# Optimization experiments

Measured on AMD Instinct MI355X. Metric: run time of the kernel, lower is better.

Reference implementation:

```python
import jax, jax.numpy as jnp
import numpy as np

DIM = 1024
HEADS = 16

def setup_inputs() -> dict:
    key = jax.random.key(0)
    k1, k2, k3, k4 = jax.random.split(key, 4)
    x = jax.random.normal(k1, (2, 2048, DIM), dtype=jnp.float32)
    # torch Linear weights are [out_features, in_features]
    w_qkv = jax.random.normal(k2, (3 * DIM, DIM), dtype=jnp.float32) * (DIM ** -0.5)
    w_out = jax.random.normal(k3, (DIM, DIM), dtype=jnp.float32) * (DIM ** -0.5)
    b_out = jax.random.normal(k4, (DIM,), dtype=jnp.float32) * 0.01
    return {"x": x, "w_qkv": w_qkv, "w_out": w_out, "b_out": b_out}

def reference(x, w_qkv, w_out, b_out):
    b, n, dim = x.shape
    h = HEADS
    d = dim // h
    scale = dim ** -0.5  # NOTE: full dim, faithful to source
    qkv = x @ w_qkv.T                       # [b, n, 3*dim]
    qkv = qkv.reshape(b, n, 3, h, d)        # split (qkv h d)
    q, k, v = (qkv[:, :, i].transpose(0, 2, 1, 3) for i in range(3))  # [b, h, n, d]
    scores = jnp.einsum('bhid,bhjd->bhij', q, k) * scale
    weights = jax.nn.softmax(scores, axis=-1)
    out = jnp.einsum('bhij,bhjd->bhid', weights, v)  # [b, h, n, d]
    out = out.transpose(0, 2, 1, 3).reshape(b, n, dim)
    return out @ w_out.T + b_out
```

## Files before the change

kernel.cpp:

```cpp
#include <hip/hip_runtime.h>

#define DIM   1024
#define HEADS 16
#define NSEQ  2048
#define BATCH 2

typedef unsigned short u16;
typedef unsigned long long u64;
typedef __attribute__((ext_vector_type(8))) short bf16x8;
typedef __attribute__((ext_vector_type(4))) float f32x4;
typedef __attribute__((ext_vector_type(16))) float f32x16;

__device__ __forceinline__ u16 f2b(float f) {
  union { float f; unsigned u; } v; v.f = f;
  unsigned r = (v.u + 0x7fffu + ((v.u >> 16) & 1u)) >> 16;
  return (u16)r;
}

__device__ __forceinline__ void g2l16(const u16* g, u16* l) {
  __builtin_amdgcn_global_load_lds(
      (const __attribute__((address_space(1))) void*)g,
      (__attribute__((address_space(3))) void*)l, 16, 0, 0);
}

__global__ void cvt_bf16(const float* __restrict__ src, u16* __restrict__ dst,
                         int n4, int sc4, float s) {
  int i = blockIdx.x * blockDim.x + threadIdx.x;
  if (i < n4) {
    float4 f = ((const float4*)src)[i];
    float m = (i < sc4) ? s : 1.0f;
    union { u16 s[4]; u64 ll; } o;
    o.s[0] = f2b(f.x * m); o.s[1] = f2b(f.y * m);
    o.s[2] = f2b(f.z * m); o.s[3] = f2b(f.w * m);
    ((u64*)dst)[i] = o.ll;
  }
}

__global__ __launch_bounds__(256, 2)
void gemm_bt(const u16* __restrict__ A, const u16* __restrict__ Bt,
             void* __restrict__ C, const float* __restrict__ bias,
             int M, int Nc, int K, int bf16_out) {
  __shared__ u16 As[128 * 64];
  __shared__ u16 Bs[128 * 64];
  const int tid  = threadIdx.x;
  const int wave = tid >> 6, lane = tid & 63;
  const int l15  = lane & 15, quad = lane >> 4;
  const int m0 = blockIdx.y * 128, n0 = blockIdx.x * 128;
  const int wm = (wave >> 1) * 64, wn = (wave & 1) * 64;
  const int rb = wave * 32;

  f32x4 acc[4][4] = {};

  for (int kt = 0; kt < K; kt += 64) {
#pragma unroll
    for (int c = 0; c < 4; ++c) {
      int r  = rb + c * 8 + (lane >> 3);
      int ck = (lane & 7) ^ (r & 7);
      g2l16(A  + (size_t)(m0 + r) * K + kt + ck * 8, &As[(rb + c * 8) * 64]);
      g2l16(Bt + (size_t)(n0 + r) * K + kt + ck * 8, &Bs[(rb + c * 8) * 64]);
    }
    __syncthreads();
#pragma unroll
    for (int ks = 0; ks < 2; ++ks) {
      bf16x8 a[4], b[4];
      int ch = ks * 4 + quad;
#pragma unroll
      for (int i = 0; i < 4; ++i) {
        int ra  = wm + i * 16 + l15;
        a[i] = *(const bf16x8*)&As[ra * 64 + ((ch ^ (ra & 7)) << 3)];
        int rb2 = wn + i * 16 + l15;
        b[i] = *(const bf16x8*)&Bs[rb2 * 64 + ((ch ^ (rb2 & 7)) << 3)];
      }
#pragma unroll
      for (int i = 0; i < 4; ++i)
#pragma unroll
        for (int j = 0; j < 4; ++j)
          acc[i][j] = __builtin_amdgcn_mfma_f32_16x16x32_bf16(a[i], b[j], acc[i][j], 0, 0, 0);
    }
    __syncthreads();
  }

#pragma unroll
  for (int i = 0; i < 4; ++i)
#pragma unroll
    for (int j = 0; j < 4; ++j) {
      int row = m0 + wm + i * 16 + quad * 4;
      int col = n0 + wn + j * 16 + l15;
#pragma unroll
      for (int r = 0; r < 4; ++r) {
        float v = acc[i][j][r];
        if (bf16_out) ((u16*)C)[(size_t)(row + r) * Nc + col] = f2b(v);
        else          ((float*)C)[(size_t)(row + r) * Nc + col] = v + bias[col];
      }
    }
}

__global__ __launch_bounds__(256, 2)
void attn(const u16* __restrict__ qkv, u16* __restrict__ outp) {
  __shared__ u16 Ks[2][128 * 64];
  __shared__ u16 Vts[2][64 * 128];
  const int tid  = threadIdx.x;
  const int wave = tid >> 6, lane = tid & 63;
  const int l31  = lane & 31, h = lane >> 5;
  const int b = blockIdx.x >> 4, hd = blockIdx.x & 15;
  const int q0 = blockIdx.y * 128;
  const u16* base = qkv + (size_t)b * NSEQ * 3072;
  const int qoff = hd * 64, koff = DIM + hd * 64, voff = 2 * DIM + hd * 64;
  const int dc = tid & 7, j0l = (tid >> 3) * 4;
  const int vchunk = (j0l >> 4) * 2 + ((j0l >> 2) & 1);
  const int vboff  = 4 * ((j0l >> 3) & 1);

  union V4 { uint4 q; u16 s[8]; };
  union PA { unsigned w[4]; bf16x8 f; };

#pragma unroll
  for (int c = 0; c < 4; ++c) {
    int bse = wave * 32 + c * 8;
    g2l16(base + (size_t)(q0 + bse + (lane >> 3)) * 3072 + qoff + (((lane & 7) ^ ((lane >> 3) & 7)) << 3),
          &Ks[0][bse * 64]);
  }
  __syncthreads();
  bf16x8 qf[4];
  {
    int qr = wave * 32 + l31;
#pragma unroll
    for (int kd = 0; kd < 4; ++kd)
      qf[kd] = *(const bf16x8*)&Ks[0][qr * 64 + (((kd * 2 + h) ^ (qr & 7)) << 3)];
  }
  __syncthreads();

  V4 vr[4];
#pragma unroll
  for (int c = 0; c < 4; ++c) {
    int bse = wave * 32 + c * 8;
    g2l16(base + (size_t)(bse + (lane >> 3)) * 3072 + koff + (((lane & 7) ^ ((lane >> 3) & 7)) << 3),
          &Ks[0][bse * 64]);
  }
#pragma unroll
  for (int e = 0; e < 4; ++e)
    vr[e].q = *(const uint4*)(base + (size_t)(j0l + e) * 3072 + voff + dc * 8);
#pragma unroll
  for (int u = 0; u < 8; ++u) {
    int d = dc * 8 + u;
    unsigned w0 = (unsigned)vr[0].s[u] | ((unsigned)vr[1].s[u] << 16);
    unsigned w1 = (unsigned)vr[2].s[u] | ((unsigned)vr[3].s[u] << 16);
    *(u64*)&Vts[0][d * 128 + ((vchunk ^ ((d + (d >> 3)) & 15)) << 3) + vboff] =
        (u64)w0 | ((u64)w1 << 32);
  }
  __syncthreads();

  float lrun = 0.0f;
  f32x16 oacc[2] = {};

  for (int t = 0; t < 16; ++t) {
    const int pbuf = t & 1;
    if (t < 15) {
      const int j0n = (t + 1) * 128;
#pragma unroll
      for (int c = 0; c < 4; ++c) {
        int bse = wave * 32 + c * 8;
        g2l16(base + (size_t)(j0n + bse + (lane >> 3)) * 3072 + koff + (((lane & 7) ^ ((lane >> 3) & 7)) << 3),
              &Ks[pbuf ^ 1][bse * 64]);
      }
#pragma unroll
      for (int e = 0; e < 4; ++e)
        vr[e].q = *(const uint4*)(base + (size_t)(j0n + j0l + e) * 3072 + voff + dc * 8);
    }

    f32x16 sc[4] = {};
#pragma unroll
    for (int kd = 0; kd < 4; ++kd) {
      bf16x8 kb[4];
#pragma unroll
      for (int ni = 0; ni < 4; ++ni) {
        int kr = ni * 32 + l31;
        kb[ni] = *(const bf16x8*)&Ks[pbuf][kr * 64 + (((kd * 2 + h) ^ (kr & 7)) << 3)];
      }
#pragma unroll
      for (int ni = 0; ni < 4; ++ni)
        sc[ni] = __builtin_amdgcn_mfma_f32_32x32x16_bf16(kb[ni], qf[kd], sc[ni], 0, 0, 0);
    }

    PA pa[8];
#pragma unroll
    for (int ni = 0; ni < 4; ++ni) {
      f32x16 p;
#pragma unroll
      for (int r = 0; r < 16; ++r) p[r] = __builtin_amdgcn_exp2f(sc[ni][r]);
      float s0 = (p[0] + p[1]) + (p[2] + p[3]);
      float s1 = (p[4] + p[5]) + (p[6] + p[7]);
      float s2 = (p[8] + p[9]) + (p[10] + p[11]);
      float s3 = (p[12] + p[13]) + (p[14] + p[15]);
      lrun += (s0 + s1) + (s2 + s3);
#pragma unroll
      for (int ks2 = 0; ks2 < 2; ++ks2)
#pragma unroll
        for (int i = 0; i < 4; ++i) {
          unsigned lo = (__float_as_uint(p[8 * ks2 + 2 * i])     + 0x8000u) >> 16;
          unsigned hi = (__float_as_uint(p[8 * ks2 + 2 * i + 1]) + 0x8000u) & 0xFFFF0000u;
          pa[2 * ni + ks2].w[i] = lo | hi;
        }
    }

#pragma unroll
    for (int f = 0; f < 8; ++f) {
      bf16x8 vb[2];
#pragma unroll
      for (int nd = 0; nd < 2; ++nd) {
        int d = nd * 32 + l31;
        vb[nd] = *(const bf16x8*)&Vts[pbuf][d * 128 + (((2 * f + h) ^ ((d + (d >> 3)) & 15)) << 3)];
      }
#pragma unroll
      for (int nd = 0; nd < 2; ++nd)
        oacc[nd] = __builtin_amdgcn_mfma_f32_32x32x16_bf16(pa[f].f, vb[nd], oacc[nd], 0, 0, 0);
    }

    if (t < 15) {
#pragma unroll
      for (int u = 0; u < 8; ++u) {
        int d = dc * 8 + u;
        unsigned w0 = (unsigned)vr[0].s[u] | ((unsigned)vr[1].s[u] << 16);
        unsigned w1 = (unsigned)vr[2].s[u] | ((unsigned)vr[3].s[u] << 16);
        *(u64*)&Vts[pbuf ^ 1][d * 128 + ((vchunk ^ ((d + (d >> 3)) & 15)) << 3) + vboff] =
            (u64)w0 | ((u64)w1 << 32);
      }
    }
    __syncthreads();
  }

  float l = lrun + __shfl_xor(lrun, 32, 64);
  float linv = 1.0f / l;
#pragma unroll
  for (int r = 0; r < 16; ++r) {
    int rowloc = (r & 3) + 8 * (r >> 2) + 4 * h;
    float lb = __shfl(linv, rowloc, 64);
    int row = q0 + wave * 32 + rowloc;
#pragma unroll
    for (int nd = 0; nd < 2; ++nd)
      outp[((size_t)b * NSEQ + row) * DIM + hd * 64 + nd * 32 + l31] = f2b(oacc[nd][r] * lb);
  }
}

extern "C" void kernel_launch(void* const* d_in, const int* in_sizes, int n_in,
                              void* d_out, int out_size, void* d_ws, size_t ws_size,
                              hipStream_t stream) {
  const float* x     = (const float*)d_in[0];
  const float* w_qkv = (const float*)d_in[1];
  const float* w_out = (const float*)d_in[2];
  const float* b_out = (const float*)d_in[3];
  float* outp = (float*)d_out;

  u16* xb    = (u16*)d_ws;
  u16* wqkvb = xb    + (size_t)4096 * 1024;
  u16* woutb = wqkvb + (size_t)3072 * 1024;
  u16* qkvb  = woutb + (size_t)1024 * 1024;
  u16* attnb = qkvb  + (size_t)4096 * 3072;

  const float C2 = 0.03125f * 1.44269504088896340736f;

  cvt_bf16<<<4096 * 1024 / 4 / 256, 256, 0, stream>>>(x,     xb,    4096 * 1024 / 4, 0, 1.0f);
  cvt_bf16<<<3072 * 1024 / 4 / 256, 256, 0, stream>>>(w_qkv, wqkvb, 3072 * 1024 / 4,
                                                      1024 * 1024 / 4, C2);
  cvt_bf16<<<1024 * 1024 / 4 / 256, 256, 0, stream>>>(w_out, woutb, 1024 * 1024 / 4, 0, 1.0f);

  gemm_bt<<<dim3(24, 32), 256, 0, stream>>>(xb, wqkvb, qkvb, nullptr, 4096, 3072, 1024, 1);
  attn<<<dim3(32, 16), 256, 0, stream>>>(qkvb, attnb);
  gemm_bt<<<dim3(8, 32), 256, 0, stream>>>(attnb, woutb, outp, b_out, 4096, 1024, 1024, 0);
}
```

Measured before the change: 195.5 us.

## Split attention KV range across two wave groups and merge conversion kernels

The attention kernel now runs 512 threads per block, with two groups of four waves each handling half of the key/value sequence in 64-row tiles. The partial outputs and row sums are combined through shared memory at the end, which roughly doubles the waves available per block to hide latency. The three fp32-to-bf16 conversion launches are also merged into one launch to cut launch overhead. This costs a final shared-memory reduction and an extra barrier, and the 512-thread block with a minimum of 4 blocks per CU in launch bounds puts tighter limits on registers.

New measurement: 197.7 us. About the same (+1.1%).

```diff
diff --git a/kernel.cpp b/kernel.cpp
--- a/kernel.cpp
+++ b/kernel.cpp
@@ -23,17 +23,23 @@
       (__attribute__((address_space(3))) void*)l, 16, 0, 0);
 }
 
-__global__ void cvt_bf16(const float* __restrict__ src, u16* __restrict__ dst,
-                         int n4, int sc4, float s) {
+#define N4_X  (4096 * 1024 / 4)
+#define N4_W  (3072 * 1024 / 4)
+#define N4_O  (1024 * 1024 / 4)
+__global__ void cvt_all(const float* __restrict__ x, const float* __restrict__ wqkv,
+                        const float* __restrict__ wout,
+                        u16* __restrict__ xb, u16* __restrict__ wqkvb,
+                        u16* __restrict__ woutb, float s) {
   int i = blockIdx.x * blockDim.x + threadIdx.x;
-  if (i < n4) {
-    float4 f = ((const float4*)src)[i];
-    float m = (i < sc4) ? s : 1.0f;
-    union { u16 s[4]; u64 ll; } o;
-    o.s[0] = f2b(f.x * m); o.s[1] = f2b(f.y * m);
-    o.s[2] = f2b(f.z * m); o.s[3] = f2b(f.w * m);
-    ((u64*)dst)[i] = o.ll;
-  }
+  const float* src; u16* dst; int j; float m = 1.0f;
+  if (i < N4_X)            { src = x;    dst = xb;    j = i; }
+  else if (i < N4_X + N4_W){ src = wqkv; dst = wqkvb; j = i - N4_X; if (j < 1024 * 1024 / 4) m = s; }
+  else                     { src = wout; dst = woutb; j = i - N4_X - N4_W; }
+  float4 f = ((const float4*)src)[j];
+  union { u16 s[4]; u64 ll; } o;
+  o.s[0] = f2b(f.x * m); o.s[1] = f2b(f.y * m);
+  o.s[2] = f2b(f.z * m); o.s[3] = f2b(f.w * m);
+  ((u64*)dst)[j] = o.ll;
 }
 
 __global__ __launch_bounds__(256, 2)
@@ -95,57 +101,62 @@
     }
 }
 
-__global__ __launch_bounds__(256, 2)
+__global__ __launch_bounds__(512, 4)
 void attn(const u16* __restrict__ qkv, u16* __restrict__ outp) {
-  __shared__ u16 Ks[2][128 * 64];
-  __shared__ u16 Vts[2][64 * 128];
+  __shared__ u16 Ks[2][2][64 * 64];
+  __shared__ u16 Vts[2][2][64 * 64];
   const int tid  = threadIdx.x;
   const int wave = tid >> 6, lane = tid & 63;
+  const int g = wave >> 2, gw = wave & 3;
   const int l31  = lane & 31, h = lane >> 5;
   const int b = blockIdx.x >> 4, hd = blockIdx.x & 15;
   const int q0 = blockIdx.y * 128;
   const u16* base = qkv + (size_t)b * NSEQ * 3072;
   const int qoff = hd * 64, koff = DIM + hd * 64, voff = 2 * DIM + hd * 64;
-  const int dc = tid & 7, j0l = (tid >> 3) * 4;
+  const int kv0 = g * 1024;
+  const int gt = tid & 255;
+  const int dc = gt & 7, j0l = (gt >> 3) * 2;
   const int vchunk = (j0l >> 4) * 2 + ((j0l >> 2) & 1);
-  const int vboff  = 4 * ((j0l >> 3) & 1);
+  const int vboff  = 4 * ((j0l >> 3) & 1) + (j0l & 3);
 
   union V4 { uint4 q; u16 s[8]; };
   union PA { unsigned w[4]; bf16x8 f; };
 
-#pragma unroll
-  for (int c = 0; c < 4; ++c) {
-    int bse = wave * 32 + c * 8;
-    g2l16(base + (size_t)(q0 + bse + (lane >> 3)) * 3072 + qoff + (((lane & 7) ^ ((lane >> 3) & 7)) << 3),
-          &Ks[0][bse * 64]);
+  u16* Kall = (u16*)Ks;
+
+#pragma unroll
+  for (int c = 0; c < 2; ++c) {
+    int bse = wave * 16 + c * 8;
+    int r = bse + (lane >> 3);
+    g2l16(base + (size_t)(q0 + r) * 3072 + qoff + (((lane & 7) ^ (r & 7)) << 3),
+          &Kall[bse * 64]);
   }
   __syncthreads();
   bf16x8 qf[4];
   {
-    int qr = wave * 32 + l31;
+    int qr = gw * 32 + l31;
 #pragma unroll
     for (int kd = 0; kd < 4; ++kd)
-      qf[kd] = *(const bf16x8*)&Ks[0][qr * 64 + (((kd * 2 + h) ^ (qr & 7)) << 3)];
-  }
-  __syncthreads();
-
-  V4 vr[4];
-#pragma unroll
-  for (int c = 0; c < 4; ++c) {
-    int bse = wave * 32 + c * 8;
-    g2l16(base + (size_t)(bse + (lane >> 3)) * 3072 + koff + (((lane & 7) ^ ((lane >> 3) & 7)) << 3),
-          &Ks[0][bse * 64]);
-  }
-#pragma unroll
-  for (int e = 0; e < 4; ++e)
-    vr[e].q = *(const uint4*)(base + (size_t)(j0l + e) * 3072 + voff + dc * 8);
+      qf[kd] = *(const bf16x8*)&Kall[qr * 64 + (((kd * 2 + h) ^ (qr & 7)) << 3)];
+  }
+  __syncthreads();
+
+  V4 vr[2];
+#pragma unroll
+  for (int c = 0; c < 2; ++c) {
+    int bse = gw * 16 + c * 8;
+    int r = bse + (lane >> 3);
+    g2l16(base + (size_t)(kv0 + r) * 3072 + koff + (((lane & 7) ^ (r & 7)) << 3),
+          &Ks[g][0][bse * 64]);
+  }
+#pragma unroll
+  for (int e = 0; e < 2; ++e)
+    vr[e].q = *(const uint4*)(base + (size_t)(kv0 + j0l + e) * 3072 + voff + dc * 8);
 #pragma unroll
   for (int u = 0; u < 8; ++u) {
     int d = dc * 8 + u;
     unsigned w0 = (unsigned)vr[0].s[u] | ((unsigned)vr[1].s[u] << 16);
-    unsigned w1 = (unsigned)vr[2].s[u] | ((unsigned)vr[3].s[u] << 16);
-    *(u64*)&Vts[0][d * 128 + ((vchunk ^ ((d + (d >> 3)) & 15)) << 3) + vboff] =
-        (u64)w0 | ((u64)w1 << 32);
+    *(unsigned*)&Vts[g][0][d * 64 + ((vchunk ^ ((d + (d >> 3)) & 7)) << 3) + vboff] = w0;
   }
   __syncthreads();
 
@@ -155,35 +166,36 @@
   for (int t = 0; t < 16; ++t) {
     const int pbuf = t & 1;
     if (t < 15) {
-      const int j0n = (t + 1) * 128;
-#pragma unroll
-      for (int c = 0; c < 4; ++c) {
-        int bse = wave * 32 + c * 8;
-        g2l16(base + (size_t)(j0n + bse + (lane >> 3)) * 3072 + koff + (((lane & 7) ^ ((lane >> 3) & 7)) << 3),
-              &Ks[pbuf ^ 1][bse * 64]);
-      }
-#pragma unroll
-      for (int e = 0; e < 4; ++e)
+      const int j0n = kv0 + (t + 1) * 64;
+#pragma unroll
+      for (int c = 0; c < 2; ++c) {
+        int bse = gw * 16 + c * 8;
+        int r = bse + (lane >> 3);
+        g2l16(base + (size_t)(j0n + r) * 3072 + koff + (((lane & 7) ^ (r & 7)) << 3),
+              &Ks[g][pbuf ^ 1][bse * 64]);
+      }
+#pragma unroll
+      for (int e = 0; e < 2; ++e)
         vr[e].q = *(const uint4*)(base + (size_t)(j0n + j0l + e) * 3072 + voff + dc * 8);
     }
 
-    f32x16 sc[4] = {};
+    f32x16 sc[2] = {};
 #pragma unroll
     for (int kd = 0; kd < 4; ++kd) {
-      bf16x8 kb[4];
-#pragma unroll
-      for (int ni = 0; ni < 4; ++ni) {
+      bf16x8 kb[2];
+#pragma unroll
+      for (int ni = 0; ni < 2; ++ni) {
         int kr = ni * 32 + l31;
-        kb[ni] = *(const bf16x8*)&Ks[pbuf][kr * 64 + (((kd * 2 + h) ^ (kr & 7)) << 3)];
-      }
-#pragma unroll
-      for (int ni = 0; ni < 4; ++ni)
+        kb[ni] = *(const bf16x8*)&Ks[g][pbuf][kr * 64 + (((kd * 2 + h) ^ (kr & 7)) << 3)];
+      }
+#pragma unroll
+      for (int ni = 0; ni < 2; ++ni)
         sc[ni] = __builtin_amdgcn_mfma_f32_32x32x16_bf16(kb[ni], qf[kd], sc[ni], 0, 0, 0);
     }
 
-    PA pa[8];
-#pragma unroll
-    for (int ni = 0; ni < 4; ++ni) {
+    PA pa[4];
+#pragma unroll
+    for (int ni = 0; ni < 2; ++ni) {
       f32x16 p;
 #pragma unroll
       for (int r = 0; r < 16; ++r) p[r] = __builtin_amdgcn_exp2f(sc[ni][r]);
@@ -203,12 +215,12 @@
     }
 
 #pragma unroll
-    for (int f = 0; f < 8; ++f) {
+    for (int f = 0; f < 4; ++f) {
       bf16x8 vb[2];
 #pragma unroll
       for (int nd = 0; nd < 2; ++nd) {
         int d = nd * 32 + l31;
-        vb[nd] = *(const bf16x8*)&Vts[pbuf][d * 128 + (((2 * f + h) ^ ((d + (d >> 3)) & 15)) << 3)];
+        vb[nd] = *(const bf16x8*)&Vts[g][pbuf][d * 64 + (((2 * f + h) ^ ((d + (d >> 3)) & 7)) << 3)];
       }
 #pragma unroll
       for (int nd = 0; nd < 2; ++nd)
@@ -220,24 +232,38 @@
       for (int u = 0; u < 8; ++u) {
         int d = dc * 8 + u;
         unsigned w0 = (unsigned)vr[0].s[u] | ((unsigned)vr[1].s[u] << 16);
-        unsigned w1 = (unsigned)vr[2].s[u] | ((unsigned)vr[3].s[u] << 16);
-        *(u64*)&Vts[pbuf ^ 1][d * 128 + ((vchunk ^ ((d + (d >> 3)) & 15)) << 3) + vboff] =
-            (u64)w0 | ((u64)w1 << 32);
+        *(unsigned*)&Vts[g][pbuf ^ 1][d * 64 + ((vchunk ^ ((d + (d >> 3)) & 7)) << 3) + vboff] = w0;
       }
     }
     __syncthreads();
   }
 
-  float l = lrun + __shfl_xor(lrun, 32, 64);
-  float linv = 1.0f / l;
-#pragma unroll
-  for (int r = 0; r < 16; ++r) {
-    int rowloc = (r & 3) + 8 * (r >> 2) + 4 * h;
-    float lb = __shfl(linv, rowloc, 64);
-    int row = q0 + wave * 32 + rowloc;
+  float* osh = (float*)Ks;
+  float* lsh = (float*)Vts;
+  if (g == 1) {
 #pragma unroll
     for (int nd = 0; nd < 2; ++nd)
-      outp[((size_t)b * NSEQ + row) * DIM + hd * 64 + nd * 32 + l31] = f2b(oacc[nd][r] * lb);
+#pragma unroll
+      for (int r = 0; r < 16; ++r)
+        osh[gw * 2048 + (nd * 16 + r) * 64 + lane] = oacc[nd][r];
+    lsh[gw * 64 + lane] = lrun;
+  }
+  __syncthreads();
+  if (g == 0) {
+    float lr = lrun + lsh[gw * 64 + lane];
+    float l = lr + __shfl_xor(lr, 32, 64);
+    float linv = 1.0f / l;
+#pragma unroll
+    for (int r = 0; r < 16; ++r) {
+      int rowloc = (r & 3) + 8 * (r >> 2) + 4 * h;
+      float lb = __shfl(linv, rowloc, 64);
+      int row = q0 + gw * 32 + rowloc;
+#pragma unroll
+      for (int nd = 0; nd < 2; ++nd) {
+        float o = oacc[nd][r] + osh[gw * 2048 + (nd * 16 + r) * 64 + lane];
+        outp[((size_t)b * NSEQ + row) * DIM + hd * 64 + nd * 32 + l31] = f2b(o * lb);
+      }
+    }
   }
 }
 
@@ -258,12 +284,10 @@
 
   const float C2 = 0.03125f * 1.44269504088896340736f;
 
-  cvt_bf16<<<4096 * 1024 / 4 / 256, 256, 0, stream>>>(x,     xb,    4096 * 1024 / 4, 0, 1.0f);
-  cvt_bf16<<<3072 * 1024 / 4 / 256, 256, 0, stream>>>(w_qkv, wqkvb, 3072 * 1024 / 4,
-                                                      1024 * 1024 / 4, C2);
-  cvt_bf16<<<1024 * 1024 / 4 / 256, 256, 0, stream>>>(w_out, woutb, 1024 * 1024 / 4, 0, 1.0f);
+  cvt_all<<<(N4_X + N4_W + N4_O) / 256, 256, 0, stream>>>(x, w_qkv, w_out,
+                                                          xb, wqkvb, woutb, C2);
 
   gemm_bt<<<dim3(24, 32), 256, 0, stream>>>(xb, wqkvb, qkvb, nullptr, 4096, 3072, 1024, 1);
-  attn<<<dim3(32, 16), 256, 0, stream>>>(qkvb, attnb);
+  attn<<<dim3(32, 16), 512, 0, stream>>>(qkvb, attnb);
   gemm_bt<<<dim3(8, 32), 256, 0, stream>>>(attnb, woutb, outp, b_out, 4096, 1024, 1024, 0);
 }
```
